# Optimization experiments

Hardware: AMD Instinct MI355X
Metric: run time of the kernel (lower is better)

## Reference

```python
import jax, jax.numpy as jnp
import numpy as np

B, N, C, H, KHOP = 8, 1024, 512, 16, 2
HD = C // H
VALID = 768          # valid (non-padded) nodes per batch row
E = B * VALID * 32   # ~deg 32 per valid node
BN_EPS = 1e-5
LN_EPS = 1e-5


def setup_inputs() -> dict:
    key = jax.random.key(0)
    ks = jax.random.split(key, 12)
    x = jax.random.normal(ks[0], (B, N, C), jnp.float32)
    shift = jax.random.normal(ks[1], (B, C), jnp.float32) * 0.1
    scale = jax.random.normal(ks[2], (B, C), jnp.float32) * 0.1
    # fixed-size valid prefix per row -> static shapes under jit
    mask = jnp.broadcast_to(jnp.arange(N) < VALID, (B, N))
    # edges live inside a single graph (same batch row), only among valid nodes,
    # expressed directly in flattened [B*N] index space (== compacted indexing up to relabeling)
    eb = jax.random.randint(ks[3], (E,), 0, B)
    es = jax.random.randint(ks[4], (E,), 0, VALID)
    ed = jax.random.randint(ks[5], (E,), 0, VALID)
    edge_index = jnp.stack([eb * N + es, eb * N + ed]).astype(jnp.int32)
    w = lambda k, s: jax.random.normal(k, s, jnp.float32) * 0.02
    gin_eps = jnp.zeros((KHOP,), jnp.float32)
    gin_w1 = w(ks[6], (KHOP, C, 2 * C)); gin_b1 = jnp.zeros((KHOP, 2 * C), jnp.float32)
    gin_bn_g = jnp.ones((KHOP, 2 * C), jnp.float32); gin_bn_b = jnp.zeros((KHOP, 2 * C), jnp.float32)
    gin_w2 = w(ks[7], (KHOP, 2 * C, C)); gin_b2 = jnp.zeros((KHOP, C), jnp.float32)
    ln_g = jnp.ones((C,), jnp.float32); ln_b = jnp.zeros((C,), jnp.float32)
    qkv_w = w(ks[8], (C, 3 * C)); qkv_b = jnp.zeros((3 * C,), jnp.float32)
    proj_w = w(ks[9], (C, C)); proj_b = jnp.zeros((C,), jnp.float32)
    return dict(x=x, shift=shift, scale=scale, mask=mask, edge_index=edge_index,
                gin_eps=gin_eps, gin_w1=gin_w1, gin_b1=gin_b1, gin_bn_g=gin_bn_g,
                gin_bn_b=gin_bn_b, gin_w2=gin_w2, gin_b2=gin_b2, ln_g=ln_g, ln_b=ln_b,
                qkv_w=qkv_w, qkv_b=qkv_b, proj_w=proj_w, proj_b=proj_b)


def _gin_layer(h, mask_f, cnt, src, dst, eps, w1, b1, g, bt, w2, b2):
    # GINConv: mlp((1+eps)*x_i + sum_{j->i} x_j); MLP = Linear->BatchNorm(batch stats over valid nodes)->ReLU->Linear
    agg = jax.ops.segment_sum(h[src], dst, num_segments=B * N)  # scatter-add messages
    z = (1.0 + eps) * h + agg
    pre = z @ w1 + b1                              # [B*N, 2C]
    mw = mask_f[:, None]
    mean = (pre * mw).sum(0) / cnt                 # masked BN statistics (valid nodes only)
    var = (((pre - mean) ** 2) * mw).sum(0) / cnt  # biased var, as torch BatchNorm
    hn = jax.nn.relu(g * (pre - mean) * jax.lax.rsqrt(var + BN_EPS) + bt)
    return (hn @ w2 + b2) * mw                     # zero out padded nodes (x_struct stays 0 there)


def reference(x, shift, scale, mask, edge_index, gin_eps, gin_w1, gin_b1, gin_bn_g,
              gin_bn_b, gin_w2, gin_b2, ln_g, ln_b, qkv_w, qkv_b, proj_w, proj_b):
    xf = x.reshape(B * N, C)
    mask_f = mask.reshape(-1).astype(x.dtype)
    cnt = mask_f.sum()
    src, dst = edge_index[0], edge_index[1]
    # structure extractor: k-hop GIN with residual after the first hop
    h = _gin_layer(xf * mask_f[:, None], mask_f, cnt, src, dst, gin_eps[0],
                   gin_w1[0], gin_b1[0], gin_bn_g[0], gin_bn_b[0], gin_w2[0], gin_b2[0])
    for i in range(1, KHOP):
        h = _gin_layer(h, mask_f, cnt, src, dst, gin_eps[i],
                       gin_w1[i], gin_b1[i], gin_bn_g[i], gin_bn_b[i], gin_w2[i], gin_b2[i]) + h
    xs = x + h.reshape(B, N, C)  # x + x_struct (x_struct zero on padded nodes)
    # LayerNorm + modulate
    mu = xs.mean(-1, keepdims=True)
    va = xs.var(-1, keepdims=True)
    xn = (xs - mu) * jax.lax.rsqrt(va + LN_EPS) * ln_g + ln_b
    xm = xn * (1.0 + scale[:, None, :]) + shift[:, None, :]
    # SDPA attention with key padding mask
    qkv = (xm @ qkv_w + qkv_b).reshape(B, N, 3, H, HD).transpose(2, 0, 3, 1, 4)
    q, k, v = qkv[0], qkv[1], qkv[2]                       # [B,H,N,HD]
    scores = jnp.einsum('bhqd,bhkd->bhqk', q, k) * (HD ** -0.5)
    scores = scores + jnp.where(mask[:, None, None, :], 0.0, -1e9)
    attn = jax.nn.softmax(scores, axis=-1)
    out = jnp.einsum('bhqk,bhkd->bhqd', attn, v).transpose(0, 2, 1, 3).reshape(B, N, C)
    return out @ proj_w + proj_b
```

## Files before the change

kernel.cpp:

```cpp
#include <hip/hip_runtime.h>
#include <hip/hip_bf16.h>

constexpr int Bc    = 8;
constexpr int Nn    = 1024;
constexpr int Cc    = 512;
constexpr int Hh    = 16;
constexpr int HD    = 32;
constexpr int VALID = 768;
constexpr float CNT_INV = 1.0f / 6144.0f;
constexpr float BN_EPS = 1e-5f;
constexpr float LN_EPS = 1e-5f;
constexpr int ROWS = Bc * Nn;
constexpr int VROWS = Bc * VALID;
constexpr float QSCL = 0.25500526764086547f;

typedef short s16x8 __attribute__((ext_vector_type(8)));
typedef float f32x4 __attribute__((ext_vector_type(4)));

static __device__ __forceinline__ unsigned short f2bf(float f) {
    __hip_bfloat16 h = __float2bfloat16(f);
    return *reinterpret_cast<unsigned short*>(&h);
}
static __device__ __forceinline__ float bf2f(unsigned short u) {
    union { unsigned int u; float f; } c; c.u = (unsigned int)u << 16;
    return c.f;
}
static __device__ __forceinline__ float exp2_fast(float x) {
    float r; asm("v_exp_f32 %0, %1" : "=v"(r) : "v"(x)); return r;
}

static __device__ __forceinline__ int vswz(int d) {
    return ((((d >> 3) ^ (d >> 1)) & 3) << 1) | (d & 1);
}

__global__ __launch_bounds__(256) void k_wt_all(const float* __restrict__ gw1,
                                                const float* __restrict__ gw2,
                                                const float* __restrict__ qkvw,
                                                const float* __restrict__ projw,
                                                const float* __restrict__ x,
                                                unsigned short* __restrict__ w1t,
                                                unsigned short* __restrict__ w2t,
                                                unsigned short* __restrict__ qkvt,
                                                unsigned short* __restrict__ projt,
                                                unsigned short* __restrict__ xb,
                                                float* __restrict__ stats,
                                                int* __restrict__ ideg) {
    const int bi = blockIdx.x;
    if (bi >= 3072) {
        int vr4 = (bi - 3072) * 4;
        int batch = vr4 / 768;
        int row = batch * 1024 + (vr4 - batch * 768);
        size_t e = (size_t)row * 512 + threadIdx.x * 8;
        float4 a = *(const float4*)&x[e];
        float4 b = *(const float4*)&x[e + 4];
        s16x8 o;
        o[0] = (short)f2bf(a.x); o[1] = (short)f2bf(a.y);
        o[2] = (short)f2bf(a.z); o[3] = (short)f2bf(a.w);
        o[4] = (short)f2bf(b.x); o[5] = (short)f2bf(b.y);
        o[6] = (short)f2bf(b.z); o[7] = (short)f2bf(b.w);
        *(s16x8*)&xb[e] = o;
        return;
    }
    if (bi == 0) {
        for (int i = threadIdx.x; i < 4096; i += 256) stats[i] = 0.f;
    } else if (bi == 1) {
        for (int i = threadIdx.x; i < 8192; i += 256) ideg[i] = 0;
    }

    const float* W; unsigned short* Wt; int K, N, bx, by;
    if (bi < 1024) {
        int z = bi >> 9, r = bi & 511;
        W = gw1 + (size_t)z * 524288; Wt = w1t + (size_t)z * 524288;
        K = 512; N = 1024; bx = r & 31; by = r >> 5;
    } else if (bi < 2048) {
        int z = (bi - 1024) >> 9, r = (bi - 1024) & 511;
        W = gw2 + (size_t)z * 524288; Wt = w2t + (size_t)z * 524288;
        K = 1024; N = 512; bx = r & 15; by = r >> 4;
    } else if (bi < 2816) {
        int r = bi - 2048;
        W = qkvw; Wt = qkvt; K = 512; N = 1536; bx = r % 48; by = r / 48;
    } else {
        int r = bi - 2816;
        W = projw; Wt = projt; K = 512; N = 512; bx = r & 15; by = r >> 4;
    }

    __shared__ float t[32][33];
    const int k0 = by * 32, n0 = bx * 32;
    int kk = threadIdx.x >> 3, nn = (threadIdx.x & 7) * 4;
    float4 v = *(const float4*)&W[(size_t)(k0 + kk) * N + n0 + nn];
    t[kk][nn] = v.x; t[kk][nn + 1] = v.y; t[kk][nn + 2] = v.z; t[kk][nn + 3] = v.w;
    __syncthreads();
    int nn2 = threadIdx.x >> 3, kk2 = (threadIdx.x & 7) * 4;
    ushort4 o;
    o.x = f2bf(t[kk2][nn2]);     o.y = f2bf(t[kk2 + 1][nn2]);
    o.z = f2bf(t[kk2 + 2][nn2]); o.w = f2bf(t[kk2 + 3][nn2]);
    *(ushort4*)&Wt[(size_t)(n0 + nn2) * K + k0 + kk2] = o;
}

__global__ __launch_bounds__(256) void k_count(const int* __restrict__ ei,
                                               int* __restrict__ deg, int E) {
    int e = blockIdx.x * 256 + threadIdx.x;
    if (e < E) atomicAdd(&deg[ei[E + e]], 1);
}

__global__ __launch_bounds__(1024) void k_scan(const int* __restrict__ deg,
                                               int* __restrict__ start,
                                               int* __restrict__ cursor) {
    __shared__ int csum[1024];
    const int t = threadIdx.x;
    const int base = t * 8;
    int local[8];
    int s = 0;
#pragma unroll
    for (int i = 0; i < 8; ++i) { local[i] = deg[base + i]; s += local[i]; }
    csum[t] = s;
    __syncthreads();
    for (int off = 1; off < 1024; off <<= 1) {
        int v = (t >= off) ? csum[t - off] : 0;
        __syncthreads();
        if (t >= off) csum[t] += v;
        __syncthreads();
    }
    int excl = (t == 0) ? 0 : csum[t - 1];
#pragma unroll
    for (int i = 0; i < 8; ++i) {
        start[base + i]  = excl;
        cursor[base + i] = excl;
        excl += local[i];
    }
    if (t == 1023) start[8192] = excl;
}

__global__ __launch_bounds__(256) void k_fill(const int* __restrict__ ei,
                                              int* __restrict__ cursor,
                                              int* __restrict__ list, int E) {
    int e = blockIdx.x * 256 + threadIdx.x;
    if (e < E) {
        int pos = atomicAdd(&cursor[ei[E + e]], 1);
        list[pos] = ei[e];
    }
}

__global__ __launch_bounds__(64) void k_gather_z(const unsigned short* __restrict__ h,
                                                 const int* __restrict__ start,
                                                 const int* __restrict__ list,
                                                 const float* __restrict__ epsArr,
                                                 int layer,
                                                 unsigned short* __restrict__ z) {
    const int vr = blockIdx.x;
    const int batch = vr & 7;
    const int row = batch * 1024 + (vr >> 3);
    const int c = threadIdx.x * 8;
    const int s0 = start[row], s1 = start[row + 1];
    const float e1 = 1.0f + epsArr[layer];
    const unsigned short* hp = h + c;
    s16x8 bv = *(const s16x8*)&h[(size_t)row * 512 + c];
    float a[8];
#pragma unroll
    for (int i = 0; i < 8; ++i) a[i] = bf2f((unsigned short)bv[i]) * e1;
    int j = s0;
    for (; j + 4 <= s1; j += 4) {
        int sA = list[j], sB = list[j + 1], sC = list[j + 2], sD = list[j + 3];
        s16x8 vA = *(const s16x8*)&hp[(size_t)sA * 512];
        s16x8 vB = *(const s16x8*)&hp[(size_t)sB * 512];
        s16x8 vC = *(const s16x8*)&hp[(size_t)sC * 512];
        s16x8 vD = *(const s16x8*)&hp[(size_t)sD * 512];
#pragma unroll
        for (int i = 0; i < 8; ++i) {
            a[i] += bf2f((unsigned short)vA[i]);
            a[i] += bf2f((unsigned short)vB[i]);
            a[i] += bf2f((unsigned short)vC[i]);
            a[i] += bf2f((unsigned short)vD[i]);
        }
    }
    for (; j < s1; ++j) {
        s16x8 vA = *(const s16x8*)&hp[(size_t)list[j] * 512];
#pragma unroll
        for (int i = 0; i < 8; ++i) a[i] += bf2f((unsigned short)vA[i]);
    }
    s16x8 o;
#pragma unroll
    for (int i = 0; i < 8; ++i) o[i] = (short)f2bf(a[i]);
    *(s16x8*)&z[(size_t)row * 512 + c] = o;
}

template <bool RESIDUAL, bool STATS, bool SKIPM, bool OUTBF, bool QSCALE,
          bool RESBF, bool SKIPKV, int BNSZ>
__global__ __launch_bounds__(256) void k_gemm_bf(const unsigned short* __restrict__ A,
                                                 const unsigned short* __restrict__ Bt,
                                                 const float* __restrict__ bias,
                                                 const void* __restrict__ res,
                                                 void* __restrict__ Cd,
                                                 float* __restrict__ stats,
                                                 int K, int Nc) {
    __shared__ unsigned short Al[128 * 64];
    __shared__ unsigned short Bl[BNSZ * 64];
    constexpr int NF = BNSZ / 32;
    constexpr int NB = (BNSZ == 128) ? 4 : 2;
    const int tid  = threadIdx.x;
    const int by   = blockIdx.y;
    const int bm   = SKIPM ? ((by / 6) * 1024 + (by % 6) * 128) : (by * 128);
    const int bn   = blockIdx.x * BNSZ;
    if (SKIPKV && (by & 7) >= 6 && bn >= 512) return;
    const int wid  = tid >> 6, lane = tid & 63;
    const int wr   = wid >> 1, wc = wid & 1;
    const int lo16 = lane & 15, g = lane >> 4;

    const int sr = tid >> 1, sh = tid & 1;
    const size_t a_off = (size_t)(bm + sr) * K + sh * 32;
    const int srb = (BNSZ == 128) ? (tid >> 1) : (tid >> 2);
    const int shb = (BNSZ == 128) ? (tid & 1)  : (tid & 3);
    const size_t b_off = (size_t)(bn + srb) * K + shb * (BNSZ == 128 ? 32 : 16);

    f32x4 acc[4][NF];
#pragma unroll
    for (int m = 0; m < 4; ++m)
#pragma unroll
        for (int n = 0; n < NF; ++n) acc[m][n] = (f32x4){0.f, 0.f, 0.f, 0.f};

    const int NT = K >> 6;
    s16x8 ar[4], br[NB];
    {
        const s16x8* ap = (const s16x8*)(A + a_off);
        const s16x8* bp = (const s16x8*)(Bt + b_off);
#pragma unroll
        for (int i = 0; i < 4; ++i)  ar[i] = ap[i];
#pragma unroll
        for (int i = 0; i < NB; ++i) br[i] = bp[i];
    }

    for (int kt = 0; kt < NT; ++kt) {
        __syncthreads();
#pragma unroll
        for (int i = 0; i < 4; ++i) {
            int sl = (sh * 4 + i) ^ (sr & 7);
            *(s16x8*)&Al[sr * 64 + sl * 8] = ar[i];
        }
#pragma unroll
        for (int i = 0; i < NB; ++i) {
            int s = (BNSZ == 128) ? (shb * 4 + i) : (shb * 2 + i);
            int sl = s ^ (srb & 7);
            *(s16x8*)&Bl[srb * 64 + sl * 8] = br[i];
        }
        __syncthreads();
        if (kt + 1 < NT) {
            const s16x8* ap = (const s16x8*)(A + a_off + (size_t)(kt + 1) * 64);
            const s16x8* bp = (const s16x8*)(Bt + b_off + (size_t)(kt + 1) * 64);
#pragma unroll
            for (int i = 0; i < 4; ++i)  ar[i] = ap[i];
#pragma unroll
            for (int i = 0; i < NB; ++i) br[i] = bp[i];
        }
#pragma unroll
        for (int ks = 0; ks < 2; ++ks) {
            s16x8 af[4], bfr[NF];
#pragma unroll
            for (int m = 0; m < 4; ++m) {
                int r = wr * 64 + m * 16 + lo16;
                int sl = (ks * 4 + g) ^ (r & 7);
                af[m] = *(const s16x8*)&Al[r * 64 + sl * 8];
            }
#pragma unroll
            for (int n = 0; n < NF; ++n) {
                int r = wc * (BNSZ / 2) + n * 16 + lo16;
                int sl = (ks * 4 + g) ^ (r & 7);
                bfr[n] = *(const s16x8*)&Bl[r * 64 + sl * 8];
            }
            __builtin_amdgcn_s_setprio(1);
#pragma unroll
            for (int m = 0; m < 4; ++m)
#pragma unroll
                for (int n = 0; n < NF; ++n)
                    acc[m][n] = __builtin_amdgcn_mfma_f32_16x16x32_bf16(
                        af[m], bfr[n], acc[m][n], 0, 0, 0);
            __builtin_amdgcn_s_setprio(0);
        }
    }

#pragma unroll
    for (int n = 0; n < NF; ++n) {
        int col = bn + wc * (BNSZ / 2) + n * 16 + lo16;
        float bb = bias[col];
        bool qs = QSCALE && (col < 512);
        float s = 0.f, s2 = 0.f;
#pragma unroll
        for (int m = 0; m < 4; ++m) {
#pragma unroll
            for (int ri = 0; ri < 4; ++ri) {
                int row = bm + wr * 64 + m * 16 + g * 4 + ri;
                float v = acc[m][n][ri] + bb;
                if (STATS) { s += v; s2 += v * v; }
                if (RESIDUAL) {
                    if (RESBF)
                        v += bf2f(((const unsigned short*)res)[(size_t)row * Nc + col]);
                    else
                        v += ((const float*)res)[(size_t)row * Nc + col];
                }
                if (QSCALE && qs) v *= QSCL;
                if (OUTBF) ((unsigned short*)Cd)[(size_t)row * Nc + col] = f2bf(v);
                else       ((float*)Cd)[(size_t)row * Nc + col] = v;
            }
        }
        if (STATS) {
            s  += __shfl_xor(s, 16);  s  += __shfl_xor(s, 32);
            s2 += __shfl_xor(s2, 16); s2 += __shfl_xor(s2, 32);
            if (g == 0) {
                atomicAdd(&stats[col], s);
                atomicAdd(&stats[1024 + col], s2);
            }
        }
    }
}

__global__ __launch_bounds__(128) void k_bn_apply(const unsigned short* __restrict__ pre,
                                                  const float* __restrict__ stats,
                                                  const float* __restrict__ g,
                                                  const float* __restrict__ bt,
                                                  unsigned short* __restrict__ hn) {
    const int vr = blockIdx.x;
    const int batch = vr & 7;
    const int row = batch * 1024 + (vr >> 3);
    const int c0 = threadIdx.x * 8;
    const size_t off = (size_t)row * 1024 + c0;
    s16x8 v = *(const s16x8*)&pre[off];
    s16x8 o;
#pragma unroll
    for (int i = 0; i < 8; ++i) {
        float sm = stats[c0 + i], sq = stats[1024 + c0 + i];
        float m = sm * CNT_INV;
        float r = rsqrtf(sq * CNT_INV - m * m + BN_EPS);
        float hv = g[c0 + i] * (bf2f((unsigned short)v[i]) - m) * r + bt[c0 + i];
        o[i] = (short)f2bf(fmaxf(hv, 0.f));
    }
    *(s16x8*)&hn[off] = o;
}

__global__ __launch_bounds__(256) void k_ln_mod(const float* __restrict__ x,
                                                const unsigned short* __restrict__ h,
                                                const float* __restrict__ lg,
                                                const float* __restrict__ lb,
                                                const float* __restrict__ sc,
                                                const float* __restrict__ sh,
                                                unsigned short* __restrict__ xm) {
    int row  = blockIdx.x * 4 + (threadIdx.x >> 6);
    int lane = threadIdx.x & 63;
    const size_t base = (size_t)row * 512 + lane * 8;
    const bool val = (row & 1023) < VALID;

    float v[8];
    float4 a0 = *(const float4*)&x[base], a1 = *(const float4*)&x[base + 4];
    s16x8 hv8 = *(const s16x8*)&h[base];
    float xa[8] = {a0.x, a0.y, a0.z, a0.w, a1.x, a1.y, a1.z, a1.w};
#pragma unroll
    for (int j = 0; j < 8; ++j) {
        float hj = val ? bf2f((unsigned short)hv8[j]) : 0.f;
        v[j] = xa[j] + hj;
    }

    float s = 0.f, s2 = 0.f;
#pragma unroll
    for (int j = 0; j < 8; ++j) { s += v[j]; s2 += v[j] * v[j]; }
#pragma unroll
    for (int off = 32; off; off >>= 1) {
        s  += __shfl_xor(s, off);
        s2 += __shfl_xor(s2, off);
    }
    float mu  = s * (1.0f / 512.0f);
    float var = s2 * (1.0f / 512.0f) - mu * mu;
    float rs  = rsqrtf(var + LN_EPS);

    int c0 = lane * 8;
    int bidx = row >> 10;
    const float* scp = sc + (size_t)bidx * 512 + c0;
    const float* shp = sh + (size_t)bidx * 512 + c0;
    s16x8 o;
#pragma unroll
    for (int j = 0; j < 8; ++j) {
        float xn = (v[j] - mu) * rs * lg[c0 + j] + lb[c0 + j];
        o[j] = (short)f2bf(xn * (1.0f + scp[j]) + shp[j]);
    }
    *(s16x8*)&xm[base] = o;
}

__global__ __launch_bounds__(256) void k_attn_mfma(const unsigned short* __restrict__ qkv,
                                                   unsigned short* __restrict__ att) {
    __shared__ __align__(16) unsigned short Kl[128 * 32];
    __shared__ __align__(16) unsigned short Vt[32 * 128];
    __shared__ __align__(16) unsigned short Pl[4][16 * 128];

    const int w    = threadIdx.x >> 6;
    const int lane = threadIdx.x & 63;
    const int bh   = blockIdx.x;
    const int b    = bh >> 4, h = bh & 15;
    const int qt   = blockIdx.y;
    const int lo16 = lane & 15;
    const int g    = lane >> 4;

    const int qrowA = qt * 128 + w * 16 + lo16;
    s16x8 qfa = *(const s16x8*)&qkv[(size_t)(b * 1024 + qrowA) * 1536 + h * 32 + g * 8];
    s16x8 qfb = *(const s16x8*)&qkv[(size_t)(b * 1024 + qrowA + 64) * 1536 + h * 32 + g * 8];

    f32x4 o0a = {0.f,0.f,0.f,0.f}, o1a = {0.f,0.f,0.f,0.f};
    f32x4 o0b = {0.f,0.f,0.f,0.f}, o1b = {0.f,0.f,0.f,0.f};
    float la = 0.f, lb = 0.f;

    const size_t kvbase = (size_t)(b * 1024) * 1536 + h * 32;

    const int kr_r = threadIdx.x >> 2;
    const int kr_g = threadIdx.x & 3;
    const int vk0  = (threadIdx.x >> 2) * 2;
    const int vgg  = threadIdx.x & 3;

    s16x8 kA, kB, vA, vB;
    {
        const unsigned short* kp = &qkv[kvbase + (size_t)kr_r * 1536 + 512 + kr_g * 8];
        kA = *(const s16x8*)kp;
        kB = *(const s16x8*)(kp + (size_t)64 * 1536);
        const unsigned short* vp = &qkv[kvbase + (size_t)vk0 * 1536 + 1024 + vgg * 8];
        vA = *(const s16x8*)vp;
        vB = *(const s16x8*)(vp + 1536);
    }

    for (int kc = 0; kc < VALID; kc += 128) {
        __syncthreads();

        {
            int slot = kr_g ^ ((kr_r >> 1) & 3);
            *(s16x8*)&Kl[kr_r * 32 + slot * 8] = kA;
            int r2 = 64 + kr_r;
            slot = kr_g ^ ((r2 >> 1) & 3);
            *(s16x8*)&Kl[r2 * 32 + slot * 8] = kB;
        }
#pragma unroll
        for (int j = 0; j < 8; ++j) {
            int d = vgg * 8 + j;
            int slot = (vk0 >> 3) ^ vswz(d);
            int elem = d * 128 + slot * 8 + (vk0 & 7);
            unsigned int pack = (unsigned int)(unsigned short)vA[j] |
                                ((unsigned int)(unsigned short)vB[j] << 16);
            *(unsigned int*)&Vt[elem] = pack;
        }
        __syncthreads();

        if (kc + 128 < VALID) {
            const unsigned short* kp = &qkv[kvbase + (size_t)(kc + 128 + kr_r) * 1536 + 512 + kr_g * 8];
            kA = *(const s16x8*)kp;
            kB = *(const s16x8*)(kp + (size_t)64 * 1536);
            const unsigned short* vp = &qkv[kvbase + (size_t)(kc + 128 + vk0) * 1536 + 1024 + vgg * 8];
            vA = *(const s16x8*)vp;
            vB = *(const s16x8*)(vp + 1536);
        }

        f32x4 sc[8];
        __builtin_amdgcn_s_setprio(1);
#pragma unroll
        for (int t = 0; t < 8; ++t) {
            int r = t * 16 + lo16;
            int slot = g ^ ((r >> 1) & 3);
            s16x8 kf = *(const s16x8*)&Kl[r * 32 + slot * 8];
            f32x4 z = {0.f, 0.f, 0.f, 0.f};
            sc[t] = __builtin_amdgcn_mfma_f32_16x16x32_bf16(kf, qfa, z, 0, 0, 0);
        }
        __builtin_amdgcn_s_setprio(0);

        {
            float lsum = 0.f;
#pragma unroll
            for (int t = 0; t < 8; ++t) {
                float p0 = exp2_fast(sc[t][0]);
                float p1 = exp2_fast(sc[t][1]);
                float p2 = exp2_fast(sc[t][2]);
                float p3 = exp2_fast(sc[t][3]);
                lsum += (p0 + p1) + (p2 + p3);
                int kstart = t * 16 + g * 4;
                int slot = (kstart >> 3) ^ (lo16 & 7);
                int elem = lo16 * 128 + slot * 8 + (kstart & 7);
                unsigned int lo = (unsigned int)f2bf(p0) | ((unsigned int)f2bf(p1) << 16);
                unsigned int hi = (unsigned int)f2bf(p2) | ((unsigned int)f2bf(p3) << 16);
                uint2 pk; pk.x = lo; pk.y = hi;
                *(uint2*)&Pl[w][elem] = pk;
            }
            la += lsum;
        }

        f32x4 sd[8];
        __builtin_amdgcn_s_setprio(1);
#pragma unroll
        for (int t = 0; t < 8; ++t) {
            int r = t * 16 + lo16;
            int slot = g ^ ((r >> 1) & 3);
            s16x8 kf = *(const s16x8*)&Kl[r * 32 + slot * 8];
            f32x4 z = {0.f, 0.f, 0.f, 0.f};
            sd[t] = __builtin_amdgcn_mfma_f32_16x16x32_bf16(kf, qfb, z, 0, 0, 0);
        }
        __builtin_amdgcn_s_setprio(0);

        asm volatile("s_waitcnt lgkmcnt(0)" ::: "memory");
        __builtin_amdgcn_sched_barrier(0);

        __builtin_amdgcn_s_setprio(1);
#pragma unroll
        for (int sub = 0; sub < 4; ++sub) {
            int slotp = (sub * 4 + g) ^ (lo16 & 7);
            s16x8 pa = *(const s16x8*)&Pl[w][lo16 * 128 + slotp * 8];
            int d0 = lo16;
            s16x8 vb0 = *(const s16x8*)&Vt[d0 * 128 + (((sub * 4 + g) ^ vswz(d0)) * 8)];
            int d1 = 16 + lo16;
            s16x8 vb1 = *(const s16x8*)&Vt[d1 * 128 + (((sub * 4 + g) ^ vswz(d1)) * 8)];
            o0a = __builtin_amdgcn_mfma_f32_16x16x32_bf16(pa, vb0, o0a, 0, 0, 0);
            o1a = __builtin_amdgcn_mfma_f32_16x16x32_bf16(pa, vb1, o1a, 0, 0, 0);
        }
        __builtin_amdgcn_s_setprio(0);

        {
            float lsum = 0.f;
#pragma unroll
            for (int t = 0; t < 8; ++t) {
                float p0 = exp2_fast(sd[t][0]);
                float p1 = exp2_fast(sd[t][1]);
                float p2 = exp2_fast(sd[t][2]);
                float p3 = exp2_fast(sd[t][3]);
                lsum += (p0 + p1) + (p2 + p3);
                int kstart = t * 16 + g * 4;
                int slot = (kstart >> 3) ^ (lo16 & 7);
                int elem = lo16 * 128 + slot * 8 + (kstart & 7);
                unsigned int lo = (unsigned int)f2bf(p0) | ((unsigned int)f2bf(p1) << 16);
                unsigned int hi = (unsigned int)f2bf(p2) | ((unsigned int)f2bf(p3) << 16);
                uint2 pk; pk.x = lo; pk.y = hi;
                *(uint2*)&Pl[w][elem] = pk;
            }
            lb += lsum;
        }

        asm volatile("s_waitcnt lgkmcnt(0)" ::: "memory");
        __builtin_amdgcn_sched_barrier(0);

        __builtin_amdgcn_s_setprio(1);
#pragma unroll
        for (int sub = 0; sub < 4; ++sub) {
            int slotp = (sub * 4 + g) ^ (lo16 & 7);
            s16x8 pa = *(const s16x8*)&Pl[w][lo16 * 128 + slotp * 8];
            int d0 = lo16;
            s16x8 vb0 = *(const s16x8*)&Vt[d0 * 128 + (((sub * 4 + g) ^ vswz(d0)) * 8)];
            int d1 = 16 + lo16;
            s16x8 vb1 = *(const s16x8*)&Vt[d1 * 128 + (((sub * 4 + g) ^ vswz(d1)) * 8)];
            o0b = __builtin_amdgcn_mfma_f32_16x16x32_bf16(pa, vb0, o0b, 0, 0, 0);
            o1b = __builtin_amdgcn_mfma_f32_16x16x32_bf16(pa, vb1, o1b, 0, 0, 0);
        }
        __builtin_amdgcn_s_setprio(0);
    }

#pragma unroll
    for (int qi = 0; qi < 2; ++qi) {
        float l = qi ? lb : la;
        l += __shfl_xor(l, 16);
        l += __shfl_xor(l, 32);
#pragma unroll
        for (int r = 0; r < 4; ++r) {
            float lr = __shfl(l, g * 4 + r);
            float inv = 1.f / lr;
            int qq = qt * 128 + qi * 64 + w * 16 + g * 4 + r;
            unsigned short* op = att + ((size_t)(b * 1024 + qq) * 512 + h * 32);
            float v0 = (qi ? o0b[r] : o0a[r]) * inv;
            float v1 = (qi ? o1b[r] : o1a[r]) * inv;
            op[lo16]      = f2bf(v0);
            op[16 + lo16] = f2bf(v1);
        }
    }
}

extern "C" void kernel_launch(void* const* d_in, const int* in_sizes, int n_in,
                              void* d_out, int out_size, void* d_ws, size_t ws_size,
                              hipStream_t stream) {
    const float* x     = (const float*)d_in[0];
    const float* shift = (const float*)d_in[1];
    const float* scale = (const float*)d_in[2];
    const int*   ei    = (const int*)d_in[4];
    const float* geps  = (const float*)d_in[5];
    const float* gw1   = (const float*)d_in[6];
    const float* gb1   = (const float*)d_in[7];
    const float* gbg   = (const float*)d_in[8];
    const float* gbb   = (const float*)d_in[9];
    const float* gw2   = (const float*)d_in[10];
    const float* gb2   = (const float*)d_in[11];
    const float* lng   = (const float*)d_in[12];
    const float* lnb   = (const float*)d_in[13];
    const float* qkvw  = (const float*)d_in[14];
    const float* qkvb  = (const float*)d_in[15];
    const float* projw = (const float*)d_in[16];
    const float* projb = (const float*)d_in[17];
    const int E = in_sizes[4] / 2;

    float* ws    = (float*)d_ws;
    float* preq  = ws + 8388608;
    float* stats = ws + 20971520;
    int*   ideg    = (int*)(ws + 20975616);
    int*   istart  = ideg + 8192;
    int*   icursor = istart + 8193;
    int*   ilist   = icursor + 8192;
    unsigned short* hnb = (unsigned short*)(ws + 16777216);
    unsigned short* wts = (unsigned short*)(ws + 21200896);
    unsigned short* w1t   = wts;
    unsigned short* w2t   = wts + 1048576;
    unsigned short* qkvt  = wts + 2097152;
    unsigned short* projt = wts + 2883584;
    unsigned short* xb   = (unsigned short*)preq;
    unsigned short* pre  = (unsigned short*)preq;
    unsigned short* zb0  = (unsigned short*)(ws + 4194304);
    unsigned short* hb   = (unsigned short*)(ws + 6291456);
    unsigned short* zb1  = (unsigned short*)ws;
    unsigned short* h2b  = (unsigned short*)(ws + 2097152);
    unsigned short* xmb  = (unsigned short*)(ws + 4194304);
    unsigned short* qkvb16 = (unsigned short*)preq;
    unsigned short* attb = (unsigned short*)ws;

    k_wt_all<<<4608, 256, 0, stream>>>(gw1, gw2, qkvw, projw, x,
                                       w1t, w2t, qkvt, projt, xb, stats, ideg);

    k_count<<<(E + 255) / 256, 256, 0, stream>>>(ei, ideg, E);
    k_scan<<<1, 1024, 0, stream>>>(ideg, istart, icursor);
    k_fill<<<(E + 255) / 256, 256, 0, stream>>>(ei, icursor, ilist, E);

    for (int layer = 0; layer < 2; ++layer) {
        const unsigned short* hin = layer ? hb : xb;
        unsigned short* zb = layer ? zb1 : zb0;
        float* st = stats + layer * 2048;
        k_gather_z<<<VROWS, 64, 0, stream>>>(hin, istart, ilist, geps, layer, zb);
        k_gemm_bf<false, true, true, true, false, false, false, 64>
            <<<dim3(16, 48), 256, 0, stream>>>(
            zb, w1t + (size_t)layer * 524288, gb1 + layer * 1024, nullptr,
            pre, st, 512, 1024);
        k_bn_apply<<<VROWS, 128, 0, stream>>>(pre, st, gbg + layer * 1024,
                                              gbb + layer * 1024, hnb);
        if (layer == 0) {
            k_gemm_bf<false, false, true, true, false, false, false, 64>
                <<<dim3(8, 48), 256, 0, stream>>>(
                hnb, w2t, gb2, nullptr, hb, nullptr, 1024, 512);
        } else {
            k_gemm_bf<true, false, true, true, false, true, false, 64>
                <<<dim3(8, 48), 256, 0, stream>>>(
                hnb, w2t + 524288, gb2 + 512, hb, h2b, nullptr, 1024, 512);
        }
    }

    k_ln_mod<<<2048, 256, 0, stream>>>(x, h2b, lng, lnb, scale, shift, xmb);
    k_gemm_bf<false, false, false, true, true, false, true, 128>
        <<<dim3(12, 64), 256, 0, stream>>>(
        xmb, qkvt, qkvb, nullptr, qkvb16, nullptr, 512, 1536);
    k_attn_mfma<<<dim3(128, 8), 256, 0, stream>>>(qkvb16, attb);
    k_gemm_bf<false, false, false, false, false, false, false, 64>
        <<<dim3(8, 64), 256, 0, stream>>>(
        attb, projt, projb, nullptr, (float*)d_out, nullptr, 512, 512);
}
```

Measured before the change: 212.9 us.

## Split attention keys across two blocks and merge partials in projection GEMM

The attention kernel now splits the 768 valid keys into two halves processed by separate blocks, doubling the grid. Each block writes unnormalized bf16 partial outputs and per-head row sums, and double-buffers its K/V LDS tiles so the next chunk's stores overlap compute. The projection GEMM gains a MERGEA mode that adds the two partials and divides by the summed normalizers while staging A into LDS. This raises attention occupancy and parallelism, at the cost of extra partial-output traffic, more LDS per block, and extra ALU work in the GEMM A-load path. Merging without per-half max rescaling relies on the existing softmax path never subtracting a row max.

Result: slower. 224.7 us (+5.5%).

```diff
diff --git a/kernel.cpp b/kernel.cpp
--- a/kernel.cpp
+++ b/kernel.cpp
@@ -185,8 +185,11 @@
 }
 
 template <bool RESIDUAL, bool STATS, bool SKIPM, bool OUTBF, bool QSCALE,
-          bool RESBF, bool SKIPKV, int BNSZ>
+          bool RESBF, bool SKIPKV, bool MERGEA, int BNSZ>
 __global__ __launch_bounds__(256) void k_gemm_bf(const unsigned short* __restrict__ A,
+                                                 const unsigned short* __restrict__ A1,
+                                                 const float* __restrict__ ls0,
+                                                 const float* __restrict__ ls1,
                                                  const unsigned short* __restrict__ Bt,
                                                  const float* __restrict__ bias,
                                                  const void* __restrict__ res,
@@ -219,22 +222,44 @@
         for (int n = 0; n < NF; ++n) acc[m][n] = (f32x4){0.f, 0.f, 0.f, 0.f};
 
     const int NT = K >> 6;
-    s16x8 ar[4], br[NB];
+    s16x8 ar[4], ar2[4], br[NB];
+    float l0v = 0.f, l1v = 0.f;
     {
         const s16x8* ap = (const s16x8*)(A + a_off);
         const s16x8* bp = (const s16x8*)(Bt + b_off);
 #pragma unroll
         for (int i = 0; i < 4; ++i)  ar[i] = ap[i];
+        if (MERGEA) {
+            const s16x8* aq = (const s16x8*)(A1 + a_off);
+#pragma unroll
+            for (int i = 0; i < 4; ++i) ar2[i] = aq[i];
+            l0v = ls0[(size_t)(bm + sr) * 16 + sh];
+            l1v = ls1[(size_t)(bm + sr) * 16 + sh];
+        }
 #pragma unroll
         for (int i = 0; i < NB; ++i) br[i] = bp[i];
     }
 
     for (int kt = 0; kt < NT; ++kt) {
         __syncthreads();
-#pragma unroll
-        for (int i = 0; i < 4; ++i) {
-            int sl = (sh * 4 + i) ^ (sr & 7);
-            *(s16x8*)&Al[sr * 64 + sl * 8] = ar[i];
+        if (MERGEA) {
+            float inv = 1.f / (l0v + l1v);
+#pragma unroll
+            for (int i = 0; i < 4; ++i) {
+                s16x8 t_;
+#pragma unroll
+                for (int j2 = 0; j2 < 8; ++j2)
+                    t_[j2] = (short)f2bf((bf2f((unsigned short)ar[i][j2]) +
+                                          bf2f((unsigned short)ar2[i][j2])) * inv);
+                int sl = (sh * 4 + i) ^ (sr & 7);
+                *(s16x8*)&Al[sr * 64 + sl * 8] = t_;
+            }
+        } else {
+#pragma unroll
+            for (int i = 0; i < 4; ++i) {
+                int sl = (sh * 4 + i) ^ (sr & 7);
+                *(s16x8*)&Al[sr * 64 + sl * 8] = ar[i];
+            }
         }
 #pragma unroll
         for (int i = 0; i < NB; ++i) {
@@ -248,6 +273,14 @@
             const s16x8* bp = (const s16x8*)(Bt + b_off + (size_t)(kt + 1) * 64);
 #pragma unroll
             for (int i = 0; i < 4; ++i)  ar[i] = ap[i];
+            if (MERGEA) {
+                const s16x8* aq = (const s16x8*)(A1 + a_off + (size_t)(kt + 1) * 64);
+#pragma unroll
+                for (int i = 0; i < 4; ++i) ar2[i] = aq[i];
+                int head = (kt + 1) * 2 + sh;
+                l0v = ls0[(size_t)(bm + sr) * 16 + head];
+                l1v = ls1[(size_t)(bm + sr) * 16 + head];
+            }
 #pragma unroll
             for (int i = 0; i < NB; ++i) br[i] = bp[i];
         }
@@ -382,15 +415,19 @@
     *(s16x8*)&xm[base] = o;
 }
 
-__global__ __launch_bounds__(256) void k_attn_mfma(const unsigned short* __restrict__ qkv,
-                                                   unsigned short* __restrict__ att) {
-    __shared__ __align__(16) unsigned short Kl[128 * 32];
-    __shared__ __align__(16) unsigned short Vt[32 * 128];
+__global__ __launch_bounds__(256) void k_attn_mfma(
+    const unsigned short* __restrict__ qkv,
+    unsigned short* __restrict__ att0,
+    unsigned short* __restrict__ att1,
+    float* __restrict__ lsum) {
+    __shared__ __align__(16) unsigned short Kl[2][128 * 32];
+    __shared__ __align__(16) unsigned short Vt[2][32 * 128];
     __shared__ __align__(16) unsigned short Pl[4][16 * 128];
 
     const int w    = threadIdx.x >> 6;
     const int lane = threadIdx.x & 63;
-    const int bh   = blockIdx.x;
+    const int xid  = blockIdx.x;
+    const int bh   = xid & 127, half = xid >> 7;
     const int b    = bh >> 4, h = bh & 15;
     const int qt   = blockIdx.y;
     const int lo16 = lane & 15;
@@ -405,6 +442,7 @@
     float la = 0.f, lb = 0.f;
 
     const size_t kvbase = (size_t)(b * 1024) * 1536 + h * 32;
+    const int kb0 = half * 384;
 
     const int kr_r = threadIdx.x >> 2;
     const int kr_g = threadIdx.x & 3;
@@ -413,43 +451,46 @@
 
     s16x8 kA, kB, vA, vB;
     {
-        const unsigned short* kp = &qkv[kvbase + (size_t)kr_r * 1536 + 512 + kr_g * 8];
+        const unsigned short* kp = &qkv[kvbase + (size_t)(kb0 + kr_r) * 1536 + 512 + kr_g * 8];
         kA = *(const s16x8*)kp;
         kB = *(const s16x8*)(kp + (size_t)64 * 1536);
-        const unsigned short* vp = &qkv[kvbase + (size_t)vk0 * 1536 + 1024 + vgg * 8];
+        const unsigned short* vp = &qkv[kvbase + (size_t)(kb0 + vk0) * 1536 + 1024 + vgg * 8];
         vA = *(const s16x8*)vp;
         vB = *(const s16x8*)(vp + 1536);
     }
-
-    for (int kc = 0; kc < VALID; kc += 128) {
-        __syncthreads();
-
-        {
-            int slot = kr_g ^ ((kr_r >> 1) & 3);
-            *(s16x8*)&Kl[kr_r * 32 + slot * 8] = kA;
-            int r2 = 64 + kr_r;
-            slot = kr_g ^ ((r2 >> 1) & 3);
-            *(s16x8*)&Kl[r2 * 32 + slot * 8] = kB;
-        }
+    {
+        int slot = kr_g ^ ((kr_r >> 1) & 3);
+        *(s16x8*)&Kl[0][kr_r * 32 + slot * 8] = kA;
+        int r2 = 64 + kr_r;
+        slot = kr_g ^ ((r2 >> 1) & 3);
+        *(s16x8*)&Kl[0][r2 * 32 + slot * 8] = kB;
 #pragma unroll
         for (int j = 0; j < 8; ++j) {
             int d = vgg * 8 + j;
-            int slot = (vk0 >> 3) ^ vswz(d);
-            int elem = d * 128 + slot * 8 + (vk0 & 7);
+            int sl = (vk0 >> 3) ^ vswz(d);
+            int elem = d * 128 + sl * 8 + (vk0 & 7);
             unsigned int pack = (unsigned int)(unsigned short)vA[j] |
                                 ((unsigned int)(unsigned short)vB[j] << 16);
-            *(unsigned int*)&Vt[elem] = pack;
-        }
+            *(unsigned int*)&Vt[0][elem] = pack;
+        }
+    }
+
+#pragma unroll
+    for (int ci = 0; ci < 3; ++ci) {
         __syncthreads();
 
-        if (kc + 128 < VALID) {
-            const unsigned short* kp = &qkv[kvbase + (size_t)(kc + 128 + kr_r) * 1536 + 512 + kr_g * 8];
+        if (ci < 2) {
+            int kcn = kb0 + (ci + 1) * 128;
+            const unsigned short* kp = &qkv[kvbase + (size_t)(kcn + kr_r) * 1536 + 512 + kr_g * 8];
             kA = *(const s16x8*)kp;
             kB = *(const s16x8*)(kp + (size_t)64 * 1536);
-            const unsigned short* vp = &qkv[kvbase + (size_t)(kc + 128 + vk0) * 1536 + 1024 + vgg * 8];
+            const unsigned short* vp = &qkv[kvbase + (size_t)(kcn + vk0) * 1536 + 1024 + vgg * 8];
             vA = *(const s16x8*)vp;
             vB = *(const s16x8*)(vp + 1536);
         }
+
+        const unsigned short* Kb = Kl[ci & 1];
+        const unsigned short* Vb = Vt[ci & 1];
 
         f32x4 sc[8];
         __builtin_amdgcn_s_setprio(1);
@@ -457,21 +498,21 @@
         for (int t = 0; t < 8; ++t) {
             int r = t * 16 + lo16;
             int slot = g ^ ((r >> 1) & 3);
-            s16x8 kf = *(const s16x8*)&Kl[r * 32 + slot * 8];
+            s16x8 kf = *(const s16x8*)&Kb[r * 32 + slot * 8];
             f32x4 z = {0.f, 0.f, 0.f, 0.f};
             sc[t] = __builtin_amdgcn_mfma_f32_16x16x32_bf16(kf, qfa, z, 0, 0, 0);
         }
         __builtin_amdgcn_s_setprio(0);
 
         {
-            float lsum = 0.f;
+            float lsv = 0.f;
 #pragma unroll
             for (int t = 0; t < 8; ++t) {
                 float p0 = exp2_fast(sc[t][0]);
                 float p1 = exp2_fast(sc[t][1]);
                 float p2 = exp2_fast(sc[t][2]);
                 float p3 = exp2_fast(sc[t][3]);
-                lsum += (p0 + p1) + (p2 + p3);
+                lsv += (p0 + p1) + (p2 + p3);
                 int kstart = t * 16 + g * 4;
                 int slot = (kstart >> 3) ^ (lo16 & 7);
                 int elem = lo16 * 128 + slot * 8 + (kstart & 7);
@@ -480,7 +521,7 @@
                 uint2 pk; pk.x = lo; pk.y = hi;
                 *(uint2*)&Pl[w][elem] = pk;
             }
-            la += lsum;
+            la += lsv;
         }
 
         f32x4 sd[8];
@@ -489,7 +530,7 @@
         for (int t = 0; t < 8; ++t) {
             int r = t * 16 + lo16;
             int slot = g ^ ((r >> 1) & 3);
-            s16x8 kf = *(const s16x8*)&Kl[r * 32 + slot * 8];
+            s16x8 kf = *(const s16x8*)&Kb[r * 32 + slot * 8];
             f32x4 z = {0.f, 0.f, 0.f, 0.f};
             sd[t] = __builtin_amdgcn_mfma_f32_16x16x32_bf16(kf, qfb, z, 0, 0, 0);
         }
@@ -504,23 +545,23 @@
             int slotp = (sub * 4 + g) ^ (lo16 & 7);
             s16x8 pa = *(const s16x8*)&Pl[w][lo16 * 128 + slotp * 8];
             int d0 = lo16;
-            s16x8 vb0 = *(const s16x8*)&Vt[d0 * 128 + (((sub * 4 + g) ^ vswz(d0)) * 8)];
+            s16x8 vb0 = *(const s16x8*)&Vb[d0 * 128 + (((sub * 4 + g) ^ vswz(d0)) * 8)];
             int d1 = 16 + lo16;
-            s16x8 vb1 = *(const s16x8*)&Vt[d1 * 128 + (((sub * 4 + g) ^ vswz(d1)) * 8)];
+            s16x8 vb1 = *(const s16x8*)&Vb[d1 * 128 + (((sub * 4 + g) ^ vswz(d1)) * 8)];
             o0a = __builtin_amdgcn_mfma_f32_16x16x32_bf16(pa, vb0, o0a, 0, 0, 0);
             o1a = __builtin_amdgcn_mfma_f32_16x16x32_bf16(pa, vb1, o1a, 0, 0, 0);
         }
         __builtin_amdgcn_s_setprio(0);
 
         {
-            float lsum = 0.f;
+            float lsv = 0.f;
 #pragma unroll
             for (int t = 0; t < 8; ++t) {
                 float p0 = exp2_fast(sd[t][0]);
                 float p1 = exp2_fast(sd[t][1]);
                 float p2 = exp2_fast(sd[t][2]);
                 float p3 = exp2_fast(sd[t][3]);
-                lsum += (p0 + p1) + (p2 + p3);
+                lsv += (p0 + p1) + (p2 + p3);
                 int kstart = t * 16 + g * 4;
                 int slot = (kstart >> 3) ^ (lo16 & 7);
                 int elem = lo16 * 128 + slot * 8 + (kstart & 7);
@@ -529,7 +570,7 @@
                 uint2 pk; pk.x = lo; pk.y = hi;
                 *(uint2*)&Pl[w][elem] = pk;
             }
-            lb += lsum;
+            lb += lsv;
         }
 
         asm volatile("s_waitcnt lgkmcnt(0)" ::: "memory");
@@ -541,31 +582,51 @@
             int slotp = (sub * 4 + g) ^ (lo16 & 7);
             s16x8 pa = *(const s16x8*)&Pl[w][lo16 * 128 + slotp * 8];
             int d0 = lo16;
-            s16x8 vb0 = *(const s16x8*)&Vt[d0 * 128 + (((sub * 4 + g) ^ vswz(d0)) * 8)];
+            s16x8 vb0 = *(const s16x8*)&Vb[d0 * 128 + (((sub * 4 + g) ^ vswz(d0)) * 8)];
             int d1 = 16 + lo16;
-            s16x8 vb1 = *(const s16x8*)&Vt[d1 * 128 + (((sub * 4 + g) ^ vswz(d1)) * 8)];
+            s16x8 vb1 = *(const s16x8*)&Vb[d1 * 128 + (((sub * 4 + g) ^ vswz(d1)) * 8)];
             o0b = __builtin_amdgcn_mfma_f32_16x16x32_bf16(pa, vb0, o0b, 0, 0, 0);
             o1b = __builtin_amdgcn_mfma_f32_16x16x32_bf16(pa, vb1, o1b, 0, 0, 0);
         }
         __builtin_amdgcn_s_setprio(0);
-    }
-
-#pragma unroll
-    for (int qi = 0; qi < 2; ++qi) {
-        float l = qi ? lb : la;
-        l += __shfl_xor(l, 16);
-        l += __shfl_xor(l, 32);
-#pragma unroll
-        for (int r = 0; r < 4; ++r) {
-            float lr = __shfl(l, g * 4 + r);
-            float inv = 1.f / lr;
-            int qq = qt * 128 + qi * 64 + w * 16 + g * 4 + r;
-            unsigned short* op = att + ((size_t)(b * 1024 + qq) * 512 + h * 32);
-            float v0 = (qi ? o0b[r] : o0a[r]) * inv;
-            float v1 = (qi ? o1b[r] : o1a[r]) * inv;
-            op[lo16]      = f2bf(v0);
-            op[16 + lo16] = f2bf(v1);
-        }
+
+        if (ci < 2) {
+            int pb = (ci + 1) & 1;
+            int slot = kr_g ^ ((kr_r >> 1) & 3);
+            *(s16x8*)&Kl[pb][kr_r * 32 + slot * 8] = kA;
+            int r2 = 64 + kr_r;
+            slot = kr_g ^ ((r2 >> 1) & 3);
+            *(s16x8*)&Kl[pb][r2 * 32 + slot * 8] = kB;
+#pragma unroll
+            for (int j = 0; j < 8; ++j) {
+                int d = vgg * 8 + j;
+                int sl = (vk0 >> 3) ^ vswz(d);
+                int elem = d * 128 + sl * 8 + (vk0 & 7);
+                unsigned int pack = (unsigned int)(unsigned short)vA[j] |
+                                    ((unsigned int)(unsigned short)vB[j] << 16);
+                *(unsigned int*)&Vt[pb][elem] = pack;
+            }
+        }
+    }
+
+    la += __shfl_xor(la, 16); la += __shfl_xor(la, 32);
+    lb += __shfl_xor(lb, 16); lb += __shfl_xor(lb, 32);
+    unsigned short* ao = half ? att1 : att0;
+    float* lo_ = lsum + (size_t)half * (ROWS * 16);
+#pragma unroll
+    for (int r = 0; r < 4; ++r) {
+        int qq = qt * 128 + w * 16 + g * 4 + r;
+        unsigned short* op = ao + ((size_t)(b * 1024 + qq) * 512 + h * 32);
+        op[lo16]      = f2bf(o0a[r]);
+        op[16 + lo16] = f2bf(o1a[r]);
+        unsigned short* op2 = ao + ((size_t)(b * 1024 + qq + 64) * 512 + h * 32);
+        op2[lo16]      = f2bf(o0b[r]);
+        op2[16 + lo16] = f2bf(o1b[r]);
+    }
+    if (lane < 16) {
+        int q0 = qt * 128 + w * 16 + lane;
+        lo_[(size_t)(b * 1024 + q0) * 16 + h]      = la;
+        lo_[(size_t)(b * 1024 + q0 + 64) * 16 + h] = lb;
     }
 }
 
@@ -612,7 +673,9 @@
     unsigned short* h2b  = (unsigned short*)(ws + 2097152);
     unsigned short* xmb  = (unsigned short*)(ws + 4194304);
     unsigned short* qkvb16 = (unsigned short*)preq;
-    unsigned short* attb = (unsigned short*)ws;
+    unsigned short* att0 = (unsigned short*)ws;
+    unsigned short* att1 = (unsigned short*)(ws + 2097152);
+    float* lsum = ws + 16777216;
 
     k_wt_all<<<4608, 256, 0, stream>>>(gw1, gw2, qkvw, projw, x,
                                        w1t, w2t, qkvt, projt, xb, stats, ideg);
@@ -626,29 +689,33 @@
         unsigned short* zb = layer ? zb1 : zb0;
         float* st = stats + layer * 2048;
         k_gather_z<<<VROWS, 64, 0, stream>>>(hin, istart, ilist, geps, layer, zb);
-        k_gemm_bf<false, true, true, true, false, false, false, 64>
+        k_gemm_bf<false, true, true, true, false, false, false, false, 64>
             <<<dim3(16, 48), 256, 0, stream>>>(
-            zb, w1t + (size_t)layer * 524288, gb1 + layer * 1024, nullptr,
-            pre, st, 512, 1024);
+            zb, nullptr, nullptr, nullptr, w1t + (size_t)layer * 524288,
+            gb1 + layer * 1024, nullptr, pre, st, 512, 1024);
         k_bn_apply<<<VROWS, 128, 0, stream>>>(pre, st, gbg + layer * 1024,
                                               gbb + layer * 1024, hnb);
         if (layer == 0) {
-            k_gemm_bf<false, false, true, true, false, false, false, 64>
+            k_gemm_bf<false, false, true, true, false, false, false, false, 64>
                 <<<dim3(8, 48), 256, 0, stream>>>(
-                hnb, w2t, gb2, nullptr, hb, nullptr, 1024, 512);
+                hnb, nullptr, nullptr, nullptr, w2t, gb2, nullptr, hb,
+                nullptr, 1024, 512);
         } else {
-            k_gemm_bf<true, false, true, true, false, true, false, 64>
+            k_gemm_bf<true, false, true, true, false, true, false, false, 64>
                 <<<dim3(8, 48), 256, 0, stream>>>(
-                hnb, w2t + 524288, gb2 + 512, hb, h2b, nullptr, 1024, 512);
+                hnb, nullptr, nullptr, nullptr, w2t + 524288, gb2 + 512, hb, h2b,
+                nullptr, 1024, 512);
         }
     }
 
     k_ln_mod<<<2048, 256, 0, stream>>>(x, h2b, lng, lnb, scale, shift, xmb);
-    k_gemm_bf<false, false, false, true, true, false, true, 128>
+    k_gemm_bf<false, false, false, true, true, false, true, false, 128>
         <<<dim3(12, 64), 256, 0, stream>>>(
-        xmb, qkvt, qkvb, nullptr, qkvb16, nullptr, 512, 1536);
-    k_attn_mfma<<<dim3(128, 8), 256, 0, stream>>>(qkvb16, attb);
-    k_gemm_bf<false, false, false, false, false, false, false, 64>
+        xmb, nullptr, nullptr, nullptr, qkvt, qkvb, nullptr, qkvb16,
+        nullptr, 512, 1536);
+    k_attn_mfma<<<dim3(256, 8), 256, 0, stream>>>(qkvb16, att0, att1, lsum);
+    k_gemm_bf<false, false, false, false, false, false, false, true, 64>
         <<<dim3(8, 64), 256, 0, stream>>>(
-        attb, projt, projb, nullptr, (float*)d_out, nullptr, 512, 512);
-}
+        att0, att1, lsum, lsum + ROWS * 16, projt, projb, nullptr,
+        (float*)d_out, nullptr, 512, 512);
+}
```
